# Optimization experiments

Measured on AMD Instinct MI355X. Metric: run time of the kernel, lower is better.

The kernel has to match this reference:

```python
import jax, jax.numpy as jnp
import numpy as np

N = 8192
D_IN = 128
D_HID = 256  # hard-coded nn.Linear(input_dim, 256) in the module
D_OUT = 64
BN_EPS = 1e-5
LEAKY_SLOPE = 0.01


def setup_inputs() -> dict:
    key = jax.random.key(0)
    k_h, k_a, k_wt, k_wo = jax.random.split(key, 4)
    H = jax.random.normal(k_h, (N, D_IN), dtype=jnp.float32)
    # Fixed adjacency passed to __init__; values in [0,1) so mask=ceil(A*1e-5) is {0,1}
    A = jax.random.uniform(k_a, (N, N), dtype=jnp.float32)
    bn_weight = jnp.ones((D_IN,), jnp.float32)
    bn_bias = jnp.zeros((D_IN,), jnp.float32)
    W_theta = jax.random.normal(k_wt, (D_IN, D_HID), jnp.float32) * np.float32(1.0 / np.sqrt(D_IN))
    b_theta = jnp.zeros((D_HID,), jnp.float32)
    W_out = jax.random.normal(k_wo, (D_IN, D_OUT), jnp.float32) * np.float32(1.0 / np.sqrt(D_IN))
    b_out = jnp.zeros((D_OUT,), jnp.float32)
    return {"H": H, "A": A, "bn_weight": bn_weight, "bn_bias": bn_bias,
            "W_theta": W_theta, "b_theta": b_theta, "W_out": W_out, "b_out": b_out}


def reference(H, A, bn_weight, bn_bias, W_theta, b_theta, W_out, b_out):
    # BatchNorm1d in training mode: biased batch statistics over the node dim
    mean = jnp.mean(H, axis=0)
    var = jnp.mean(jnp.square(H - mean), axis=0)
    Hn = (H - mean) * jax.lax.rsqrt(var + BN_EPS) * bn_weight + bn_bias  # [N, D_IN]

    Hx = Hn @ W_theta + b_theta  # [N, 256]
    mask = jnp.ceil(A * 1e-5)    # constant {0,1} mask from fixed adjacency

    # Dynamic adjacency: clamp(sigmoid(Hx Hx^T), min=0.1) * mask + I
    S = jnp.clip(jax.nn.sigmoid(Hx @ Hx.T), 0.1, None)  # [N, N]
    Ad = S * mask + jnp.eye(N, dtype=H.dtype)

    # D^{-1/2} A D^{-1/2} via broadcast scaling (same math as diag matmuls)
    d = jax.lax.rsqrt(jnp.sum(Ad, axis=1))  # D^{-0.5}, [N]
    A_hat = Ad * d[:, None] * d[None, :]

    out = A_hat @ (Hn @ W_out + b_out)       # [N, D_OUT]
    out = jnp.where(out >= 0, out, LEAKY_SLOPE * out)  # LeakyReLU(0.01)
    return out, A_hat
```

## Files before the change

### kernel.cpp

```cpp
#include <hip/hip_runtime.h>
#include <hip/hip_bf16.h>

#define N 8192
#define DIN 128
#define DHID 256
#define DOUT 64
#define LDP 72
#define VP 136

typedef __attribute__((ext_vector_type(8))) short short8;
typedef __attribute__((ext_vector_type(8))) unsigned short u16x8;
typedef __attribute__((ext_vector_type(4))) float f32x4;
typedef __attribute__((ext_vector_type(4))) unsigned short u16x4;

typedef __attribute__((address_space(1))) const unsigned int GlbU32;
typedef __attribute__((address_space(3))) unsigned int LdsU32;

__device__ inline void gload16(const void* g, void* l) {
  __builtin_amdgcn_global_load_lds((GlbU32*)g, (LdsU32*)l, 16, 0, 0);
}

__device__ inline unsigned short f2bf(float x) {
  unsigned u = __float_as_uint(x);
  u += 0x7FFF + ((u >> 16) & 1);
  return (unsigned short)(u >> 16);
}
__device__ inline float bf2f(unsigned short u) {
  return __uint_as_float(((unsigned)u) << 16);
}
__device__ inline float sig_clip(float x) {
  float s = 1.0f / (1.0f + __expf(-x));
  return fmaxf(s, 0.1f);
}

__global__ __launch_bounds__(256) void maskpack(const float* __restrict__ A,
                                                unsigned long long* __restrict__ Mb) {
  size_t i = (size_t)blockIdx.x * 256 + threadIdx.x;
  size_t step = (size_t)gridDim.x * 256;
  int l = threadIdx.x & 63;
  for (; i < (size_t)N * N / 4; i += step) {
    f32x4 a = *(const f32x4*)&A[i * 4];
    unsigned long long b0 = __ballot(a[0] > 0.f);
    unsigned long long b1 = __ballot(a[1] > 0.f);
    unsigned long long b2 = __ballot(a[2] > 0.f);
    unsigned long long b3 = __ballot(a[3] > 0.f);
    size_t g = (i - l) >> 6;
    if (l < 4) {
      unsigned long long bb = (l == 0) ? b0 : (l == 1) ? b1 : (l == 2) ? b2 : b3;
      Mb[g * 4 + l] = bb;
    }
  }
}

__global__ void bn_stats(const float* __restrict__ H, const float* __restrict__ bnw,
                         const float* __restrict__ bnb, float* __restrict__ scale,
                         float* __restrict__ shift) {
  int f = blockIdx.x;
  int t = threadIdx.x;
  float s = 0.f, sq = 0.f;
  for (int r = t; r < N; r += 256) {
    float v = H[(size_t)r * DIN + f];
    s += v; sq += v * v;
  }
  __shared__ float ss[256], s2[256];
  ss[t] = s; s2[t] = sq;
  __syncthreads();
  for (int o = 128; o > 0; o >>= 1) {
    if (t < o) { ss[t] += ss[t + o]; s2[t] += s2[t + o]; }
    __syncthreads();
  }
  if (t == 0) {
    float mean = ss[0] * (1.0f / N);
    float var = s2[0] * (1.0f / N) - mean * mean;
    float sc = rsqrtf(var + 1e-5f) * bnw[f];
    scale[f] = sc;
    shift[f] = bnb[f] - mean * sc;
  }
}

__global__ __launch_bounds__(256) void proj(const float* __restrict__ H,
                     const float* __restrict__ scale, const float* __restrict__ shift,
                     const float* __restrict__ Wt, const float* __restrict__ bt,
                     const float* __restrict__ Wo, const float* __restrict__ bo,
                     unsigned short* __restrict__ Hx, unsigned short* __restrict__ M2T) {
  __shared__ float hn[8][DIN];
  int i0 = blockIdx.x * 8;
  int t = threadIdx.x;
  #pragma unroll
  for (int rep = 0; rep < 4; ++rep) {
    int idx = rep * 256 + t;
    int r = idx >> 7, c = idx & 127;
    float h = H[(size_t)(i0 + r) * DIN + c];
    hn[r][c] = fmaf(h, scale[c], shift[c]);
  }
  __syncthreads();
  {
    int c = t;
    float acc[8];
    float b = bt[c];
    #pragma unroll
    for (int r = 0; r < 8; ++r) acc[r] = b;
    for (int k = 0; k < DIN; ++k) {
      float w = Wt[k * DHID + c];
      #pragma unroll
      for (int r = 0; r < 8; ++r) acc[r] = fmaf(hn[r][k], w, acc[r]);
    }
    #pragma unroll
    for (int r = 0; r < 8; ++r) Hx[(size_t)(i0 + r) * DHID + c] = f2bf(acc[r]);
  }
  if (t < DOUT) {
    int c = t;
    float acc[8];
    float b = bo[c];
    #pragma unroll
    for (int r = 0; r < 8; ++r) acc[r] = b;
    for (int k = 0; k < DIN; ++k) {
      float w = Wo[k * DOUT + c];
      #pragma unroll
      for (int r = 0; r < 8; ++r) acc[r] = fmaf(hn[r][k], w, acc[r]);
    }
    u16x8 v;
    #pragma unroll
    for (int r = 0; r < 8; ++r) v[r] = f2bf(acc[r]);
    *(u16x8*)&M2T[(size_t)c * N + i0] = v;
  }
}

template <int BF16V>
__global__ __launch_bounds__(256) void smat(const unsigned short* __restrict__ Hx,
                     const unsigned long long* __restrict__ Mb,
                     float* __restrict__ rowsum,
                     void* __restrict__ Vout) {
  __shared__ unsigned short lsh[17408];
  __shared__ unsigned mbt32[128][4];
  unsigned short* la = lsh;
  unsigned short* lb = lsh + 8192;
  int jt = blockIdx.x, it = blockIdx.y;
  int i0 = it * 128, j0 = jt * 128;
  int t = threadIdx.x;
  int w = t >> 6, l = t & 63;
  int lr = l & 15, lg = l >> 4;

  if (t < 128) {
    const unsigned long long* src = &Mb[(size_t)(i0 + t) * (N / 64) + (j0 >> 8) * 4];
    int sh = (j0 & 128) ? 32 : 0;
    #pragma unroll
    for (int e = 0; e < 4; ++e)
      mbt32[t][e] = (unsigned)(src[e] >> sh);
  }

  f32x4 acc[2][8];
  f32x4 zero = {0.f, 0.f, 0.f, 0.f};
  #pragma unroll
  for (int m = 0; m < 2; ++m)
    #pragma unroll
    for (int n = 0; n < 8; ++n) acc[m][n] = zero;

  const int srow = l >> 3;
  const int scol = ((l & 7) ^ srow) * 8;
  const int fswz = (lr & 7) * 8;

  for (int c4 = 0; c4 < 4; ++c4) {
    int k0 = c4 * 64;
    __syncthreads();
    #pragma unroll
    for (int rp = 0; rp < 4; ++rp) {
      int chunk = rp * 4 + w;
      int row = chunk * 8 + srow;
      gload16(&Hx[(size_t)(i0 + row) * DHID + k0 + scol], &la[chunk * 512]);
      gload16(&Hx[(size_t)(j0 + row) * DHID + k0 + scol], &lb[chunk * 512]);
    }
    __syncthreads();
    #pragma unroll
    for (int kk = 0; kk < 2; ++kk) {
      int c = (kk * 32 + lg * 8) ^ fswz;
      short8 af[2], bf[8];
      #pragma unroll
      for (int m = 0; m < 2; ++m)
        af[m] = *(const short8*)&la[(w * 32 + m * 16 + lr) * 64 + c];
      #pragma unroll
      for (int n = 0; n < 8; ++n)
        bf[n] = *(const short8*)&lb[(n * 16 + lr) * 64 + c];
      #pragma unroll
      for (int m = 0; m < 2; ++m)
        #pragma unroll
        for (int n = 0; n < 8; ++n)
          acc[m][n] = __builtin_amdgcn_mfma_f32_16x16x32_bf16(af[m], bf[n], acc[m][n], 0, 0, 0);
    }
  }

  if (BF16V) __syncthreads();

  #pragma unroll
  for (int m = 0; m < 2; ++m) {
    #pragma unroll
    for (int r = 0; r < 4; ++r) {
      int rl = w * 32 + m * 16 + lg * 4 + r;
      int gi = i0 + rl;
      unsigned mw = mbt32[rl][lr & 3];
      float part = 0.f;
      #pragma unroll
      for (int n = 0; n < 8; ++n) {
        int gj = j0 + n * 16 + lr;
        float ms = ((mw >> (n * 4 + (lr >> 2))) & 1u) ? 1.f : 0.f;
        float v = sig_clip(acc[m][n][r]) * ms + (gi == gj ? 1.f : 0.f);
        part += v;
        if (BF16V)
          lsh[rl * VP + n * 16 + lr] = f2bf(v);
        else
          ((float*)Vout)[(size_t)gi * N + gj] = v;
      }
      part += __shfl_xor(part, 1);
      part += __shfl_xor(part, 2);
      part += __shfl_xor(part, 4);
      part += __shfl_xor(part, 8);
      if (lr == 0) atomicAdd(&rowsum[gi], part);
    }
  }

  if (BF16V) {
    __syncthreads();
    #pragma unroll
    for (int pass = 0; pass < 8; ++pass) {
      int row = pass * 16 + (t >> 4);
      int cc = (t & 15) * 8;
      u16x8 vv = *(const u16x8*)&lsh[row * VP + cc];
      *(u16x8*)&((unsigned short*)Vout)[(size_t)(i0 + row) * N + j0 + cc] = vv;
    }
  }
}

__global__ void dfin(float* rs) {
  int i = blockIdx.x * 256 + threadIdx.x;
  if (i < N) rs[i] = rsqrtf(rs[i]);
}

template <int BF16V>
__global__ __launch_bounds__(256) void outmm(const void* __restrict__ Vin,
                      const float* __restrict__ dd,
                      const unsigned short* __restrict__ M2T,
                      float* __restrict__ Ahat, float* __restrict__ out) {
  __shared__ unsigned short la[128 * LDP];
  int kc = blockIdx.x;
  int it = blockIdx.y;
  int i0 = it * 128;
  int jbase = kc * 512;
  int t = threadIdx.x;
  int w = t >> 6, l = t & 63;
  int lr = l & 15, lg = l >> 4;

  f32x4 acc[2][4];
  f32x4 zero = {0.f, 0.f, 0.f, 0.f};
  #pragma unroll
  for (int m = 0; m < 2; ++m)
    #pragma unroll
    for (int n = 0; n < 4; ++n) acc[m][n] = zero;

  for (int s = 0; s < 8; ++s) {
    int j0 = jbase + s * 64;
    __syncthreads();
    if (BF16V) {
      #pragma unroll
      for (int rep = 0; rep < 4; ++rep) {
        int row = rep * 32 + (t >> 3);
        int cc = (t & 7) * 8;
        size_t idx = (size_t)(i0 + row) * N + j0 + cc;
        u16x8 u = *(const u16x8*)&((const unsigned short*)Vin)[idx];
        float di = dd[i0 + row];
        f32x4 dj0 = *(const f32x4*)&dd[j0 + cc];
        f32x4 dj1 = *(const f32x4*)&dd[j0 + cc + 4];
        f32x4 s0, s1;
        s0[0] = bf2f(u[0]) * di * dj0[0]; s0[1] = bf2f(u[1]) * di * dj0[1];
        s0[2] = bf2f(u[2]) * di * dj0[2]; s0[3] = bf2f(u[3]) * di * dj0[3];
        s1[0] = bf2f(u[4]) * di * dj1[0]; s1[1] = bf2f(u[5]) * di * dj1[1];
        s1[2] = bf2f(u[6]) * di * dj1[2]; s1[3] = bf2f(u[7]) * di * dj1[3];
        *(f32x4*)&Ahat[idx] = s0;
        *(f32x4*)&Ahat[idx + 4] = s1;
        u16x8 b;
        b[0] = f2bf(s0[0]); b[1] = f2bf(s0[1]); b[2] = f2bf(s0[2]); b[3] = f2bf(s0[3]);
        b[4] = f2bf(s1[0]); b[5] = f2bf(s1[1]); b[6] = f2bf(s1[2]); b[7] = f2bf(s1[3]);
        *(u16x8*)&la[row * LDP + cc] = b;
      }
    } else {
      #pragma unroll
      for (int rep = 0; rep < 8; ++rep) {
        int row = rep * 16 + (t >> 4);
        int cc = (t & 15) * 4;
        size_t idx = (size_t)(i0 + row) * N + j0 + cc;
        f32x4 v = *(const f32x4*)&((const float*)Vin)[idx];
        float di = dd[i0 + row];
        f32x4 dj = *(const f32x4*)&dd[j0 + cc];
        f32x4 sv;
        sv[0] = v[0] * di * dj[0]; sv[1] = v[1] * di * dj[1];
        sv[2] = v[2] * di * dj[2]; sv[3] = v[3] * di * dj[3];
        *(f32x4*)&Ahat[idx] = sv;
        u16x4 b;
        b[0] = f2bf(sv[0]); b[1] = f2bf(sv[1]); b[2] = f2bf(sv[2]); b[3] = f2bf(sv[3]);
        *(u16x4*)&la[row * LDP + cc] = b;
      }
    }
    __syncthreads();
    #pragma unroll
    for (int kk = 0; kk < 2; ++kk) {
      short8 af[2], bfr[4];
      #pragma unroll
      for (int m = 0; m < 2; ++m)
        af[m] = *(const short8*)&la[(w * 32 + m * 16 + lr) * LDP + kk * 32 + lg * 8];
      #pragma unroll
      for (int n = 0; n < 4; ++n)
        bfr[n] = *(const short8*)&M2T[(size_t)(n * 16 + lr) * N + j0 + kk * 32 + lg * 8];
      #pragma unroll
      for (int m = 0; m < 2; ++m)
        #pragma unroll
        for (int n = 0; n < 4; ++n)
          acc[m][n] = __builtin_amdgcn_mfma_f32_16x16x32_bf16(af[m], bfr[n], acc[m][n], 0, 0, 0);
    }
  }
  #pragma unroll
  for (int m = 0; m < 2; ++m)
    #pragma unroll
    for (int n = 0; n < 4; ++n)
      #pragma unroll
      for (int r = 0; r < 4; ++r) {
        int gi = i0 + w * 32 + m * 16 + lg * 4 + r;
        int gc = n * 16 + lr;
        atomicAdd(&out[(size_t)gi * DOUT + gc], acc[m][n][r]);
      }
}

__global__ void leaky(float* out) {
  int i = blockIdx.x * 256 + threadIdx.x;
  if (i < N * DOUT) {
    float x = out[i];
    out[i] = x >= 0.f ? x : 0.01f * x;
  }
}

extern "C" void kernel_launch(void* const* d_in, const int* in_sizes, int n_in,
                              void* d_out, int out_size, void* d_ws, size_t ws_size,
                              hipStream_t stream) {
  const float* H   = (const float*)d_in[0];
  const float* A   = (const float*)d_in[1];
  const float* bnw = (const float*)d_in[2];
  const float* bnb = (const float*)d_in[3];
  const float* Wt  = (const float*)d_in[4];
  const float* bt  = (const float*)d_in[5];
  const float* Wo  = (const float*)d_in[6];
  const float* bo  = (const float*)d_in[7];
  float* out = (float*)d_out;
  float* Ahat = out + (size_t)N * DOUT;

  char* ws = (char*)d_ws;
  float* scale  = (float*)(ws + 0);
  float* shift  = (float*)(ws + 512);
  float* rowsum = (float*)(ws + 4096);
  unsigned short* M2T = (unsigned short*)(ws + 65536);
  unsigned short* Hx  = (unsigned short*)(ws + 2097152);
  unsigned long long* Mb = (unsigned long long*)(ws + (size_t)(6u << 20));
  unsigned short* Vbf = (unsigned short*)(ws + (size_t)(14u << 20));

  const size_t need_bf16 = ((size_t)14 << 20) + (size_t)N * N * 2;
  const bool big = ws_size >= need_bf16;

  hipMemsetAsync(rowsum, 0, N * sizeof(float), stream);
  hipMemsetAsync(out, 0, (size_t)N * DOUT * sizeof(float), stream);

  maskpack<<<4096, 256, 0, stream>>>(A, Mb);
  bn_stats<<<DIN, 256, 0, stream>>>(H, bnw, bnb, scale, shift);
  proj<<<N / 8, 256, 0, stream>>>(H, scale, shift, Wt, bt, Wo, bo, Hx, M2T);
  if (big) {
    smat<1><<<dim3(64, 64), 256, 0, stream>>>(Hx, Mb, rowsum, (void*)Vbf);
    dfin<<<N / 256, 256, 0, stream>>>(rowsum);
    outmm<1><<<dim3(16, 64), 256, 0, stream>>>((const void*)Vbf, rowsum, M2T, Ahat, out);
  } else {
    smat<0><<<dim3(64, 64), 256, 0, stream>>>(Hx, Mb, rowsum, (void*)Ahat);
    dfin<<<N / 256, 256, 0, stream>>>(rowsum);
    outmm<0><<<dim3(16, 64), 256, 0, stream>>>((const void*)Ahat, rowsum, M2T, Ahat, out);
  }
  leaky<<<(N * DOUT + 255) / 256, 256, 0, stream>>>(out);
}
```

Baseline: 331.0 us.

## Double-buffer LDS and register-prefetch V tiles in outmm bf16 path

In the bf16 path of the output matmul kernel, the next 64-column tile of V is now loaded into registers while the current one is being scaled and multiplied. The LDS tile is double-buffered, so each step needs only one barrier instead of two. The M2T fragments and d_j values are also loaded ahead of the barrier. The aim is to hide global load latency behind the scaling, Ahat stores and MFMA work, at the cost of more registers, which may lower occupancy.

```diff
diff --git a/kernel.cpp b/kernel.cpp
--- a/kernel.cpp
+++ b/kernel.cpp
@@ -19,6 +19,14 @@
 __device__ inline void gload16(const void* g, void* l) {
   __builtin_amdgcn_global_load_lds((GlbU32*)g, (LdsU32*)l, 16, 0, 0);
 }
+
+#define LGKM_BAR()                                            \
+  do {                                                        \
+    asm volatile("s_waitcnt lgkmcnt(0)" ::: "memory");        \
+    __builtin_amdgcn_sched_barrier(0);                        \
+    __builtin_amdgcn_s_barrier();                             \
+    __builtin_amdgcn_sched_barrier(0);                        \
+  } while (0)
 
 __device__ inline unsigned short f2bf(float x) {
   unsigned u = __float_as_uint(x);
@@ -240,7 +248,7 @@
                       const float* __restrict__ dd,
                       const unsigned short* __restrict__ M2T,
                       float* __restrict__ Ahat, float* __restrict__ out) {
-  __shared__ unsigned short la[128 * LDP];
+  __shared__ unsigned short la[2][128 * LDP];
   int kc = blockIdx.x;
   int it = blockIdx.y;
   int i0 = it * 128;
@@ -256,66 +264,110 @@
     #pragma unroll
     for (int n = 0; n < 4; ++n) acc[m][n] = zero;
 
-  for (int s = 0; s < 8; ++s) {
-    int j0 = jbase + s * 64;
-    __syncthreads();
-    if (BF16V) {
+  if (BF16V) {
+    const unsigned short* V = (const unsigned short*)Vin;
+    const int row8 = t >> 3;
+    const int cc8 = (t & 7) * 8;
+
+    float di[4];
+    #pragma unroll
+    for (int rep = 0; rep < 4; ++rep) di[rep] = dd[i0 + rep * 32 + row8];
+
+    u16x8 u[2][4];
+    #pragma unroll
+    for (int rep = 0; rep < 4; ++rep)
+      u[0][rep] = *(const u16x8*)&V[(size_t)(i0 + rep * 32 + row8) * N + jbase + cc8];
+
+    #pragma unroll
+    for (int s = 0; s < 8; ++s) {
+      const int cur = s & 1;
+      const int j0 = jbase + s * 64;
+      if (s < 7) {
+        #pragma unroll
+        for (int rep = 0; rep < 4; ++rep)
+          u[cur ^ 1][rep] = *(const u16x8*)&V[(size_t)(i0 + rep * 32 + row8) * N + j0 + 64 + cc8];
+      }
+      short8 bfr[2][4];
+      #pragma unroll
+      for (int kk = 0; kk < 2; ++kk)
+        #pragma unroll
+        for (int n = 0; n < 4; ++n)
+          bfr[kk][n] = *(const short8*)&M2T[(size_t)(n * 16 + lr) * N + j0 + kk * 32 + lg * 8];
+      f32x4 dj0 = *(const f32x4*)&dd[j0 + cc8];
+      f32x4 dj1 = *(const f32x4*)&dd[j0 + cc8 + 4];
       #pragma unroll
       for (int rep = 0; rep < 4; ++rep) {
-        int row = rep * 32 + (t >> 3);
-        int cc = (t & 7) * 8;
-        size_t idx = (size_t)(i0 + row) * N + j0 + cc;
-        u16x8 u = *(const u16x8*)&((const unsigned short*)Vin)[idx];
-        float di = dd[i0 + row];
-        f32x4 dj0 = *(const f32x4*)&dd[j0 + cc];
-        f32x4 dj1 = *(const f32x4*)&dd[j0 + cc + 4];
+        int row = rep * 32 + row8;
+        size_t idx = (size_t)(i0 + row) * N + j0 + cc8;
         f32x4 s0, s1;
-        s0[0] = bf2f(u[0]) * di * dj0[0]; s0[1] = bf2f(u[1]) * di * dj0[1];
-        s0[2] = bf2f(u[2]) * di * dj0[2]; s0[3] = bf2f(u[3]) * di * dj0[3];
-        s1[0] = bf2f(u[4]) * di * dj1[0]; s1[1] = bf2f(u[5]) * di * dj1[1];
-        s1[2] = bf2f(u[6]) * di * dj1[2]; s1[3] = bf2f(u[7]) * di * dj1[3];
+        s0[0] = bf2f(u[cur][rep][0]) * di[rep] * dj0[0];
+        s0[1] = bf2f(u[cur][rep][1]) * di[rep] * dj0[1];
+        s0[2] = bf2f(u[cur][rep][2]) * di[rep] * dj0[2];
+        s0[3] = bf2f(u[cur][rep][3]) * di[rep] * dj0[3];
+        s1[0] = bf2f(u[cur][rep][4]) * di[rep] * dj1[0];
+        s1[1] = bf2f(u[cur][rep][5]) * di[rep] * dj1[1];
+        s1[2] = bf2f(u[cur][rep][6]) * di[rep] * dj1[2];
+        s1[3] = bf2f(u[cur][rep][7]) * di[rep] * dj1[3];
         *(f32x4*)&Ahat[idx] = s0;
         *(f32x4*)&Ahat[idx + 4] = s1;
         u16x8 b;
         b[0] = f2bf(s0[0]); b[1] = f2bf(s0[1]); b[2] = f2bf(s0[2]); b[3] = f2bf(s0[3]);
         b[4] = f2bf(s1[0]); b[5] = f2bf(s1[1]); b[6] = f2bf(s1[2]); b[7] = f2bf(s1[3]);
-        *(u16x8*)&la[row * LDP + cc] = b;
-      }
-    } else {
+        *(u16x8*)&la[cur][row * LDP + cc8] = b;
+      }
+      LGKM_BAR();
+      #pragma unroll
+      for (int kk = 0; kk < 2; ++kk) {
+        short8 af[2];
+        #pragma unroll
+        for (int m = 0; m < 2; ++m)
+          af[m] = *(const short8*)&la[cur][(w * 32 + m * 16 + lr) * LDP + kk * 32 + lg * 8];
+        #pragma unroll
+        for (int m = 0; m < 2; ++m)
+          #pragma unroll
+          for (int n = 0; n < 4; ++n)
+            acc[m][n] = __builtin_amdgcn_mfma_f32_16x16x32_bf16(af[m], bfr[kk][n], acc[m][n], 0, 0, 0);
+      }
+    }
+  } else {
+    for (int s = 0; s < 8; ++s) {
+      int j0 = jbase + s * 64;
+      __syncthreads();
       #pragma unroll
       for (int rep = 0; rep < 8; ++rep) {
         int row = rep * 16 + (t >> 4);
         int cc = (t & 15) * 4;
         size_t idx = (size_t)(i0 + row) * N + j0 + cc;
         f32x4 v = *(const f32x4*)&((const float*)Vin)[idx];
-        float di = dd[i0 + row];
+        float dii = dd[i0 + row];
         f32x4 dj = *(const f32x4*)&dd[j0 + cc];
         f32x4 sv;
-        sv[0] = v[0] * di * dj[0]; sv[1] = v[1] * di * dj[1];
-        sv[2] = v[2] * di * dj[2]; sv[3] = v[3] * di * dj[3];
+        sv[0] = v[0] * dii * dj[0]; sv[1] = v[1] * dii * dj[1];
+        sv[2] = v[2] * dii * dj[2]; sv[3] = v[3] * dii * dj[3];
         *(f32x4*)&Ahat[idx] = sv;
         u16x4 b;
         b[0] = f2bf(sv[0]); b[1] = f2bf(sv[1]); b[2] = f2bf(sv[2]); b[3] = f2bf(sv[3]);
-        *(u16x4*)&la[row * LDP + cc] = b;
-      }
-    }
-    __syncthreads();
-    #pragma unroll
-    for (int kk = 0; kk < 2; ++kk) {
-      short8 af[2], bfr[4];
-      #pragma unroll
-      for (int m = 0; m < 2; ++m)
-        af[m] = *(const short8*)&la[(w * 32 + m * 16 + lr) * LDP + kk * 32 + lg * 8];
-      #pragma unroll
-      for (int n = 0; n < 4; ++n)
-        bfr[n] = *(const short8*)&M2T[(size_t)(n * 16 + lr) * N + j0 + kk * 32 + lg * 8];
-      #pragma unroll
-      for (int m = 0; m < 2; ++m)
+        *(u16x4*)&la[0][row * LDP + cc] = b;
+      }
+      __syncthreads();
+      #pragma unroll
+      for (int kk = 0; kk < 2; ++kk) {
+        short8 af[2], bfr[4];
+        #pragma unroll
+        for (int m = 0; m < 2; ++m)
+          af[m] = *(const short8*)&la[0][(w * 32 + m * 16 + lr) * LDP + kk * 32 + lg * 8];
         #pragma unroll
         for (int n = 0; n < 4; ++n)
-          acc[m][n] = __builtin_amdgcn_mfma_f32_16x16x32_bf16(af[m], bfr[n], acc[m][n], 0, 0, 0);
-    }
-  }
+          bfr[n] = *(const short8*)&M2T[(size_t)(n * 16 + lr) * N + j0 + kk * 32 + lg * 8];
+        #pragma unroll
+        for (int m = 0; m < 2; ++m)
+          #pragma unroll
+          for (int n = 0; n < 4; ++n)
+            acc[m][n] = __builtin_amdgcn_mfma_f32_16x16x32_bf16(af[m], bfr[n], acc[m][n], 0, 0, 0);
+      }
+    }
+  }
+
   #pragma unroll
   for (int m = 0; m < 2; ++m)
     #pragma unroll
```

After: 333.0 us. No clear change (+0.6%).

## Exploit symmetry of Hx·Hxᵀ and split normalization from the PV matmul

Applied to the files above, without the earlier changes.

The S-matrix kernel now computes only upper-triangular tiles and writes the mirrored tile transposed, using the transposed mask bits and atomically adding column sums into the row sums. This roughly halves the MFMA and sigmoid work. The D^-1/2 scaling is factored out of the aggregation: M2T is pre-scaled by d_j, the PV matmul loads the raw bf16 V through async global-to-LDS loads and scales by d_i at the end, and a separate pass writes the fp32 A_hat. The fp32 fallback path for small workspaces is removed, so the kernel assumes the large workspace is always available, and bf16 rounding of M2T·d_j adds slight numeric differences.

```diff
diff --git a/kernel.cpp b/kernel.cpp
--- a/kernel.cpp
+++ b/kernel.cpp
@@ -5,13 +5,11 @@
 #define DIN 128
 #define DHID 256
 #define DOUT 64
-#define LDP 72
 #define VP 136
 
 typedef __attribute__((ext_vector_type(8))) short short8;
 typedef __attribute__((ext_vector_type(8))) unsigned short u16x8;
 typedef __attribute__((ext_vector_type(4))) float f32x4;
-typedef __attribute__((ext_vector_type(4))) unsigned short u16x4;
 
 typedef __attribute__((address_space(1))) const unsigned int GlbU32;
 typedef __attribute__((address_space(3))) unsigned int LdsU32;
@@ -126,20 +124,23 @@
   }
 }
 
-template <int BF16V>
 __global__ __launch_bounds__(256) void smat(const unsigned short* __restrict__ Hx,
                      const unsigned long long* __restrict__ Mb,
                      float* __restrict__ rowsum,
-                     void* __restrict__ Vout) {
+                     unsigned short* __restrict__ Vout) {
+  int jt = blockIdx.x, it = blockIdx.y;
+  if (jt < it) return;
   __shared__ unsigned short lsh[17408];
   __shared__ unsigned mbt32[128][4];
+  __shared__ unsigned mbtT[128][4];
+  __shared__ float scs[4][128];
   unsigned short* la = lsh;
   unsigned short* lb = lsh + 8192;
-  int jt = blockIdx.x, it = blockIdx.y;
   int i0 = it * 128, j0 = jt * 128;
   int t = threadIdx.x;
   int w = t >> 6, l = t & 63;
   int lr = l & 15, lg = l >> 4;
+  const bool offdiag = (it != jt);
 
   if (t < 128) {
     const unsigned long long* src = &Mb[(size_t)(i0 + t) * (N / 64) + (j0 >> 8) * 4];
@@ -147,6 +148,13 @@
     #pragma unroll
     for (int e = 0; e < 4; ++e)
       mbt32[t][e] = (unsigned)(src[e] >> sh);
+  }
+  if (offdiag && t < 128) {
+    const unsigned long long* srcT = &Mb[(size_t)(j0 + t) * (N / 64) + (i0 >> 8) * 4];
+    int shT = (i0 & 128) ? 32 : 0;
+    #pragma unroll
+    for (int e = 0; e < 4; ++e)
+      mbtT[t][e] = (unsigned)(srcT[e] >> shT);
   }
 
   f32x4 acc[2][8];
@@ -189,7 +197,7 @@
     }
   }
 
-  if (BF16V) __syncthreads();
+  __syncthreads();
 
   #pragma unroll
   for (int m = 0; m < 2; ++m) {
@@ -205,10 +213,7 @@
         float ms = ((mw >> (n * 4 + (lr >> 2))) & 1u) ? 1.f : 0.f;
         float v = sig_clip(acc[m][n][r]) * ms + (gi == gj ? 1.f : 0.f);
         part += v;
-        if (BF16V)
-          lsh[rl * VP + n * 16 + lr] = f2bf(v);
-        else
-          ((float*)Vout)[(size_t)gi * N + gj] = v;
+        lsh[rl * VP + n * 16 + lr] = f2bf(v);
       }
       part += __shfl_xor(part, 1);
       part += __shfl_xor(part, 2);
@@ -218,14 +223,56 @@
     }
   }
 
-  if (BF16V) {
-    __syncthreads();
+  __syncthreads();
+  #pragma unroll
+  for (int pass = 0; pass < 8; ++pass) {
+    int row = pass * 16 + (t >> 4);
+    int cc = (t & 15) * 8;
+    u16x8 vv = *(const u16x8*)&lsh[row * VP + cc];
+    *(u16x8*)&Vout[(size_t)(i0 + row) * N + j0 + cc] = vv;
+  }
+
+  if (offdiag) {
+    __syncthreads();
+    float p[8];
+    #pragma unroll
+    for (int n = 0; n < 8; ++n) p[n] = 0.f;
+    #pragma unroll
+    for (int m = 0; m < 2; ++m) {
+      #pragma unroll
+      for (int r = 0; r < 4; ++r) {
+        int rl = w * 32 + m * 16 + lg * 4 + r;
+        int bitp = w * 8 + m * 4 + lg;
+        #pragma unroll
+        for (int n = 0; n < 8; ++n) {
+          int c = n * 16 + lr;
+          float ms = ((mbtT[c][r] >> bitp) & 1u) ? 1.f : 0.f;
+          float v = sig_clip(acc[m][n][r]) * ms;
+          p[n] += v;
+          lsh[c * VP + rl] = f2bf(v);
+        }
+      }
+    }
+    #pragma unroll
+    for (int n = 0; n < 8; ++n) {
+      p[n] += __shfl_xor(p[n], 16);
+      p[n] += __shfl_xor(p[n], 32);
+    }
+    if (lg == 0) {
+      #pragma unroll
+      for (int n = 0; n < 8; ++n) scs[w][n * 16 + lr] = p[n];
+    }
+    __syncthreads();
+    if (t < 128) {
+      float cs = scs[0][t] + scs[1][t] + scs[2][t] + scs[3][t];
+      atomicAdd(&rowsum[j0 + t], cs);
+    }
     #pragma unroll
     for (int pass = 0; pass < 8; ++pass) {
       int row = pass * 16 + (t >> 4);
       int cc = (t & 15) * 8;
       u16x8 vv = *(const u16x8*)&lsh[row * VP + cc];
-      *(u16x8*)&((unsigned short*)Vout)[(size_t)(i0 + row) * N + j0 + cc] = vv;
+      *(u16x8*)&Vout[(size_t)(j0 + row) * N + i0 + cc] = vv;
     }
   }
 }
@@ -235,19 +282,36 @@
   if (i < N) rs[i] = rsqrtf(rs[i]);
 }
 
-template <int BF16V>
-__global__ __launch_bounds__(256) void outmm(const void* __restrict__ Vin,
-                      const float* __restrict__ dd,
-                      const unsigned short* __restrict__ M2T,
-                      float* __restrict__ Ahat, float* __restrict__ out) {
-  __shared__ unsigned short la[128 * LDP];
+__global__ __launch_bounds__(256) void m2scale(unsigned short* __restrict__ M2T,
+                                               const float* __restrict__ dd) {
+  int idx = blockIdx.x * 256 + threadIdx.x;
+  int c = idx >> 10;
+  int j8 = (idx & 1023) * 8;
+  u16x8 v = *(u16x8*)&M2T[(size_t)c * N + j8];
+  f32x4 d0 = *(const f32x4*)&dd[j8];
+  f32x4 d1 = *(const f32x4*)&dd[j8 + 4];
+  u16x8 o;
+  o[0] = f2bf(bf2f(v[0]) * d0[0]); o[1] = f2bf(bf2f(v[1]) * d0[1]);
+  o[2] = f2bf(bf2f(v[2]) * d0[2]); o[3] = f2bf(bf2f(v[3]) * d0[3]);
+  o[4] = f2bf(bf2f(v[4]) * d1[0]); o[5] = f2bf(bf2f(v[5]) * d1[1]);
+  o[6] = f2bf(bf2f(v[6]) * d1[2]); o[7] = f2bf(bf2f(v[7]) * d1[3]);
+  *(u16x8*)&M2T[(size_t)c * N + j8] = o;
+}
+
+__global__ __launch_bounds__(256) void pvmm(const unsigned short* __restrict__ V,
+                     const float* __restrict__ dd,
+                     const unsigned short* __restrict__ M2Ts,
+                     float* __restrict__ out) {
+  __shared__ unsigned short lv[8192];
   int kc = blockIdx.x;
   int it = blockIdx.y;
   int i0 = it * 128;
-  int jbase = kc * 512;
   int t = threadIdx.x;
   int w = t >> 6, l = t & 63;
   int lr = l & 15, lg = l >> 4;
+  const int srow = l >> 3;
+  const int scol = ((l & 7) ^ srow) * 8;
+  const int fswz = (lr & 7) * 8;
 
   f32x4 acc[2][4];
   f32x4 zero = {0.f, 0.f, 0.f, 0.f};
@@ -257,58 +321,25 @@
     for (int n = 0; n < 4; ++n) acc[m][n] = zero;
 
   for (int s = 0; s < 8; ++s) {
-    int j0 = jbase + s * 64;
-    __syncthreads();
-    if (BF16V) {
-      #pragma unroll
-      for (int rep = 0; rep < 4; ++rep) {
-        int row = rep * 32 + (t >> 3);
-        int cc = (t & 7) * 8;
-        size_t idx = (size_t)(i0 + row) * N + j0 + cc;
-        u16x8 u = *(const u16x8*)&((const unsigned short*)Vin)[idx];
-        float di = dd[i0 + row];
-        f32x4 dj0 = *(const f32x4*)&dd[j0 + cc];
-        f32x4 dj1 = *(const f32x4*)&dd[j0 + cc + 4];
-        f32x4 s0, s1;
-        s0[0] = bf2f(u[0]) * di * dj0[0]; s0[1] = bf2f(u[1]) * di * dj0[1];
-        s0[2] = bf2f(u[2]) * di * dj0[2]; s0[3] = bf2f(u[3]) * di * dj0[3];
-        s1[0] = bf2f(u[4]) * di * dj1[0]; s1[1] = bf2f(u[5]) * di * dj1[1];
-        s1[2] = bf2f(u[6]) * di * dj1[2]; s1[3] = bf2f(u[7]) * di * dj1[3];
-        *(f32x4*)&Ahat[idx] = s0;
-        *(f32x4*)&Ahat[idx + 4] = s1;
-        u16x8 b;
-        b[0] = f2bf(s0[0]); b[1] = f2bf(s0[1]); b[2] = f2bf(s0[2]); b[3] = f2bf(s0[3]);
-        b[4] = f2bf(s1[0]); b[5] = f2bf(s1[1]); b[6] = f2bf(s1[2]); b[7] = f2bf(s1[3]);
-        *(u16x8*)&la[row * LDP + cc] = b;
-      }
-    } else {
-      #pragma unroll
-      for (int rep = 0; rep < 8; ++rep) {
-        int row = rep * 16 + (t >> 4);
-        int cc = (t & 15) * 4;
-        size_t idx = (size_t)(i0 + row) * N + j0 + cc;
-        f32x4 v = *(const f32x4*)&((const float*)Vin)[idx];
-        float di = dd[i0 + row];
-        f32x4 dj = *(const f32x4*)&dd[j0 + cc];
-        f32x4 sv;
-        sv[0] = v[0] * di * dj[0]; sv[1] = v[1] * di * dj[1];
-        sv[2] = v[2] * di * dj[2]; sv[3] = v[3] * di * dj[3];
-        *(f32x4*)&Ahat[idx] = sv;
-        u16x4 b;
-        b[0] = f2bf(sv[0]); b[1] = f2bf(sv[1]); b[2] = f2bf(sv[2]); b[3] = f2bf(sv[3]);
-        *(u16x4*)&la[row * LDP + cc] = b;
-      }
+    int j0 = kc * 512 + s * 64;
+    __syncthreads();
+    #pragma unroll
+    for (int rp = 0; rp < 4; ++rp) {
+      int chunk = rp * 4 + w;
+      int row = chunk * 8 + srow;
+      gload16(&V[(size_t)(i0 + row) * N + j0 + scol], &lv[chunk * 512]);
     }
     __syncthreads();
     #pragma unroll
     for (int kk = 0; kk < 2; ++kk) {
+      int c = (kk * 32 + lg * 8) ^ fswz;
       short8 af[2], bfr[4];
       #pragma unroll
       for (int m = 0; m < 2; ++m)
-        af[m] = *(const short8*)&la[(w * 32 + m * 16 + lr) * LDP + kk * 32 + lg * 8];
+        af[m] = *(const short8*)&lv[(w * 32 + m * 16 + lr) * 64 + c];
       #pragma unroll
       for (int n = 0; n < 4; ++n)
-        bfr[n] = *(const short8*)&M2T[(size_t)(n * 16 + lr) * N + j0 + kk * 32 + lg * 8];
+        bfr[n] = *(const short8*)&M2Ts[(size_t)(n * 16 + lr) * N + j0 + kk * 32 + lg * 8];
       #pragma unroll
       for (int m = 0; m < 2; ++m)
         #pragma unroll
@@ -316,16 +347,40 @@
           acc[m][n] = __builtin_amdgcn_mfma_f32_16x16x32_bf16(af[m], bfr[n], acc[m][n], 0, 0, 0);
     }
   }
+
   #pragma unroll
   for (int m = 0; m < 2; ++m)
     #pragma unroll
-    for (int n = 0; n < 4; ++n)
-      #pragma unroll
-      for (int r = 0; r < 4; ++r) {
-        int gi = i0 + w * 32 + m * 16 + lg * 4 + r;
-        int gc = n * 16 + lr;
-        atomicAdd(&out[(size_t)gi * DOUT + gc], acc[m][n][r]);
-      }
+    for (int r = 0; r < 4; ++r) {
+      int gi = i0 + w * 32 + m * 16 + lg * 4 + r;
+      float di = dd[gi];
+      #pragma unroll
+      for (int n = 0; n < 4; ++n)
+        atomicAdd(&out[(size_t)gi * DOUT + n * 16 + lr], di * acc[m][n][r]);
+    }
+}
+
+__global__ __launch_bounds__(256) void ascale(const unsigned short* __restrict__ V,
+                                              const float* __restrict__ dd,
+                                              float* __restrict__ Ahat) {
+  int row = blockIdx.x;
+  float di = dd[row];
+  const unsigned short* vr = V + (size_t)row * N;
+  float* ar = Ahat + (size_t)row * N;
+  #pragma unroll
+  for (int itr = 0; itr < 4; ++itr) {
+    int c0 = (itr * 256 + threadIdx.x) * 8;
+    u16x8 v = *(const u16x8*)&vr[c0];
+    f32x4 dj0 = *(const f32x4*)&dd[c0];
+    f32x4 dj1 = *(const f32x4*)&dd[c0 + 4];
+    f32x4 o0, o1;
+    o0[0] = bf2f(v[0]) * di * dj0[0]; o0[1] = bf2f(v[1]) * di * dj0[1];
+    o0[2] = bf2f(v[2]) * di * dj0[2]; o0[3] = bf2f(v[3]) * di * dj0[3];
+    o1[0] = bf2f(v[4]) * di * dj1[0]; o1[1] = bf2f(v[5]) * di * dj1[1];
+    o1[2] = bf2f(v[6]) * di * dj1[2]; o1[3] = bf2f(v[7]) * di * dj1[3];
+    *(f32x4*)&ar[c0] = o0;
+    *(f32x4*)&ar[c0 + 4] = o1;
+  }
 }
 
 __global__ void leaky(float* out) {
@@ -359,23 +414,16 @@
   unsigned long long* Mb = (unsigned long long*)(ws + (size_t)(6u << 20));
   unsigned short* Vbf = (unsigned short*)(ws + (size_t)(14u << 20));
 
-  const size_t need_bf16 = ((size_t)14 << 20) + (size_t)N * N * 2;
-  const bool big = ws_size >= need_bf16;
-
   hipMemsetAsync(rowsum, 0, N * sizeof(float), stream);
   hipMemsetAsync(out, 0, (size_t)N * DOUT * sizeof(float), stream);
 
   maskpack<<<4096, 256, 0, stream>>>(A, Mb);
   bn_stats<<<DIN, 256, 0, stream>>>(H, bnw, bnb, scale, shift);
   proj<<<N / 8, 256, 0, stream>>>(H, scale, shift, Wt, bt, Wo, bo, Hx, M2T);
-  if (big) {
-    smat<1><<<dim3(64, 64), 256, 0, stream>>>(Hx, Mb, rowsum, (void*)Vbf);
-    dfin<<<N / 256, 256, 0, stream>>>(rowsum);
-    outmm<1><<<dim3(16, 64), 256, 0, stream>>>((const void*)Vbf, rowsum, M2T, Ahat, out);
-  } else {
-    smat<0><<<dim3(64, 64), 256, 0, stream>>>(Hx, Mb, rowsum, (void*)Ahat);
-    dfin<<<N / 256, 256, 0, stream>>>(rowsum);
-    outmm<0><<<dim3(16, 64), 256, 0, stream>>>((const void*)Ahat, rowsum, M2T, Ahat, out);
-  }
+  smat<<<dim3(64, 64), 256, 0, stream>>>(Hx, Mb, rowsum, Vbf);
+  dfin<<<N / 256, 256, 0, stream>>>(rowsum);
+  m2scale<<<256, 256, 0, stream>>>(M2T, rowsum);
+  pvmm<<<dim3(16, 64), 256, 0, stream>>>(Vbf, rowsum, M2T, out);
+  ascale<<<N, 256, 0, stream>>>(Vbf, rowsum, Ahat);
   leaky<<<(N * DOUT + 255) / 256, 256, 0, stream>>>(out);
 }
```

Measured after the change: 359.7 us. 1.09x slower.
